# Kernel tuning notes

Hardware: AMD Instinct MI355X
Metric: run time of the kernel (lower is better)

## Reference

```python
import jax, jax.numpy as jnp
import numpy as np

N_NODES = 50000
N_EDGES = 800000
D_IN = 128
D_OUT = 128


def setup_inputs() -> dict:
    key = jax.random.key(0)
    k1, k2, k3, k4, k5, k6 = jax.random.split(key, 6)
    curr_fea = jax.random.normal(k1, (N_NODES, D_IN), dtype=jnp.float32)
    edge_index = jax.random.randint(k2, (2, N_EDGES), 0, N_NODES, dtype=jnp.int64)
    s = 1.0 / np.sqrt(D_IN)
    W_self = jax.random.uniform(k3, (D_OUT, D_IN), jnp.float32, -s, s)
    b_self = jax.random.uniform(k4, (D_OUT,), jnp.float32, -s, s)
    W_neig = jax.random.uniform(k5, (D_OUT, D_IN), jnp.float32, -s, s)
    b_neig = jax.random.uniform(k6, (D_OUT,), jnp.float32, -s, s)
    return {"curr_fea": curr_fea, "edge_index": edge_index,
            "W_self": W_self, "b_self": b_self,
            "W_neig": W_neig, "b_neig": b_neig}


def reference(curr_fea, edge_index, W_self, b_self, W_neig, b_neig):
    num_nodes = curr_fea.shape[0]
    src, dst = edge_index[0], edge_index[1]
    # symmetrize: messages flow both directions
    src_all = jnp.concatenate([src, dst], axis=0)  # [2E]
    dst_all = jnp.concatenate([dst, src], axis=0)  # [2E]
    # gather neighbor features then scatter-add into destination nodes
    nei_sum = jax.ops.segment_sum(curr_fea[src_all], dst_all,
                                  num_segments=num_nodes)  # [N, d]
    out = (curr_fea @ W_self.T + b_self) + (nei_sum @ W_neig.T + b_neig)
    return out
```

## Files before the change

kernel.cpp:

```cpp
#include <hip/hip_runtime.h>

#define DD 128
#define BM 64
#define BK 32
#define BKN 64
#define NBMAX 1024
#define ECH 2048
#define CAP 2304

typedef __attribute__((ext_vector_type(8))) short bf16x8;
typedef __attribute__((ext_vector_type(4))) float f32x4;

__device__ __forceinline__ unsigned short f2b(float x) {
    unsigned u = __float_as_uint(x);
    u += 0x7fffu + ((u >> 16) & 1u);
    return (unsigned short)(u >> 16);
}
__device__ __forceinline__ float b2f_lo(unsigned v) { return __uint_as_float(v << 16); }
__device__ __forceinline__ float b2f_hi(unsigned v) { return __uint_as_float(v & 0xffff0000u); }
__device__ __forceinline__ float bf(unsigned short u) {
    return __uint_as_float((unsigned)u << 16);
}

__device__ __forceinline__ int detect_rf(const void* ei_raw, int E, int lane) {
    const unsigned long long* p = (const unsigned long long*)ei_raw;
    int n64 = E < 64 ? E : 64;
    bool big = (lane < n64) && (p[lane] >= (1ULL << 32));
    return (__ballot(big) == 0ULL) ? 1 : 0;
}

__global__ void detect_kernel(const unsigned long long* __restrict__ ei,
                              int n64, int* __restrict__ flag) {
    int i = threadIdx.x;
    bool big = (i < n64) && (ei[i] >= (1ULL << 32));
    unsigned long long b = __ballot(big);
    if (i == 0) *flag = (b == 0ULL) ? 1 : 0;
}

__global__ void cvt_all_kernel(const float* __restrict__ fea,
                               const float* __restrict__ Ws,
                               const float* __restrict__ Wn,
                               unsigned short* __restrict__ feaB,
                               unsigned short* __restrict__ Wcat, int n4) {
    int i = blockIdx.x * 256 + threadIdx.x;
    if (i < n4) {
        float4 v = reinterpret_cast<const float4*>(fea)[i];
        ushort4 o;
        o.x = f2b(v.x); o.y = f2b(v.y); o.z = f2b(v.z); o.w = f2b(v.w);
        reinterpret_cast<ushort4*>(feaB)[i] = o;
    } else if (i < n4 + 2 * DD * DD / 4) {
        int k4 = i - n4;
        int n = k4 >> 6;
        int kk = (k4 & 63) * 4;
        float4 v = (kk < DD) ? *reinterpret_cast<const float4*>(Ws + n * DD + kk)
                             : *reinterpret_cast<const float4*>(Wn + n * DD + kk - DD);
        ushort4 o;
        o.x = f2b(v.x); o.y = f2b(v.y); o.z = f2b(v.z); o.w = f2b(v.w);
        reinterpret_cast<ushort4*>(Wcat)[k4] = o;
    }
}

__global__ void cvt_fea_kernel(const float* __restrict__ in,
                               unsigned short* __restrict__ out, int n4) {
    int i = blockIdx.x * 256 + threadIdx.x;
    if (i >= n4) return;
    float4 v = reinterpret_cast<const float4*>(in)[i];
    ushort4 o;
    o.x = f2b(v.x); o.y = f2b(v.y); o.z = f2b(v.z); o.w = f2b(v.w);
    reinterpret_cast<ushort4*>(out)[i] = o;
}

__global__ void cvt_w_kernel(const float* __restrict__ Ws,
                             const float* __restrict__ Wn,
                             unsigned short* __restrict__ Wcat) {
    int i = blockIdx.x * 256 + threadIdx.x;
    int n = i >> 8, k = i & 255;
    float v = (k < DD) ? Ws[n * DD + k] : Wn[n * DD + (k - DD)];
    Wcat[i] = f2b(v);
}

__launch_bounds__(512)
__global__ void bin_kernel(const void* __restrict__ ei_raw, int E,
                           unsigned* __restrict__ region,
                           unsigned* __restrict__ gcur, int nbk) {
    __shared__ unsigned stage[2 * ECH];
    __shared__ unsigned cnt[NBMAX];
    __shared__ unsigned start[NBMAX];
    __shared__ unsigned cursor[NBMAX];
    __shared__ unsigned gbase[NBMAX];
    __shared__ unsigned scanT[512];

    const int t = threadIdx.x;
    const int lane = t & 63;
    const int rf = detect_rf(ei_raw, E, lane);

    for (int b = t; b < NBMAX; b += 512) { cnt[b] = 0; cursor[b] = 0; }
    __syncthreads();

    const int e0 = blockIdx.x * ECH;
    int es[4], ed[4];
#pragma unroll
    for (int j = 0; j < 4; ++j) {
        int e = e0 + j * 512 + t;
        if (e < E) {
            if (rf) {
                const long long* p = (const long long*)ei_raw;
                es[j] = (int)p[e]; ed[j] = (int)p[e + E];
            } else {
                const int* p = (const int*)ei_raw;
                es[j] = p[e]; ed[j] = p[e + E];
            }
            atomicAdd(&cnt[ed[j] >> 6], 1u);
            atomicAdd(&cnt[es[j] >> 6], 1u);
        } else {
            es[j] = -1; ed[j] = -1;
        }
    }
    __syncthreads();

    unsigned lv[2]; unsigned lsum = 0;
#pragma unroll
    for (int j = 0; j < 2; ++j) { lv[j] = cnt[t * 2 + j]; lsum += lv[j]; }
    scanT[t] = lsum; __syncthreads();
    for (int o = 1; o < 512; o <<= 1) {
        unsigned x = (t >= o) ? scanT[t - o] : 0;
        __syncthreads();
        scanT[t] += x;
        __syncthreads();
    }
    unsigned run = scanT[t] - lsum;
#pragma unroll
    for (int j = 0; j < 2; ++j) { start[t * 2 + j] = run; run += lv[j]; }
    __syncthreads();

#pragma unroll
    for (int j = 0; j < 4; ++j) {
        if (es[j] >= 0) {
            int s = es[j], d = ed[j];
            unsigned p0 = atomicAdd(&cursor[d >> 6], 1u);
            stage[start[d >> 6] + p0] = (unsigned)(d & 63) | ((unsigned)s << 6);
            unsigned p1 = atomicAdd(&cursor[s >> 6], 1u);
            stage[start[s >> 6] + p1] = (unsigned)(s & 63) | ((unsigned)d << 6);
        }
    }
    __syncthreads();

    for (int b = t; b < nbk; b += 512) {
        unsigned c = cnt[b];
        gbase[b] = c ? atomicAdd(&gcur[b], c) : 0;
    }
    __syncthreads();

    const int w = t >> 6;
    for (int b = w; b < nbk; b += 8) {
        unsigned c = cnt[b];
        if (!c) continue;
        unsigned gb = gbase[b], st = start[b];
        for (unsigned l2 = lane; l2 < c; l2 += 64) {
            unsigned idx = gb + l2;
            if (idx < CAP)
                region[(size_t)b * CAP + idx] = stage[st + l2];
        }
    }
}

__launch_bounds__(512)
__global__ void gather_sort_kernel(const unsigned short* __restrict__ feaB,
                                   const unsigned* __restrict__ region,
                                   const unsigned* __restrict__ gcur,
                                   unsigned short* __restrict__ neiB, int M) {
    __shared__ unsigned ent[CAP];
    __shared__ unsigned srt[CAP];
    __shared__ unsigned c64[BKN];
    __shared__ unsigned p64[BKN + 1];
    __shared__ unsigned cur64[BKN];

    const int t = threadIdx.x, b = blockIdx.x;
    unsigned cnt = gcur[b];
    if (cnt > CAP) cnt = CAP;
    const unsigned* reg = region + (size_t)b * CAP;

    for (unsigned i = t; i < cnt; i += 512) ent[i] = reg[i];
    if (t < BKN) { c64[t] = 0; cur64[t] = 0; }
    __syncthreads();

    for (unsigned i = t; i < cnt; i += 512) atomicAdd(&c64[ent[i] & 63u], 1u);
    __syncthreads();

    if (t == 0) {
        unsigned r = 0;
        for (int n = 0; n < BKN; ++n) { p64[n] = r; r += c64[n]; }
        p64[BKN] = r;
    }
    __syncthreads();

    for (unsigned i = t; i < cnt; i += 512) {
        unsigned e = ent[i];
        unsigned p = atomicAdd(&cur64[e & 63u], 1u);
        srt[p64[e & 63u] + p] = e >> 6;
    }
    __syncthreads();

    const int w = t >> 6, lane = t & 63;
    const int half = lane >> 5, li = lane & 31;
    const unsigned short* bp = feaB + li * 4;

    for (int n = w; n < BKN; n += 8) {
        int g = b * BKN + n;
        if (g >= M) break;
        unsigned p = p64[n], d = c64[n];
        float a0 = 0.f, a1 = 0.f, a2 = 0.f, a3 = 0.f;
        unsigned j = 0;
        for (; j + 8 <= d; j += 8) {
            unsigned s0 = srt[p + j + half];
            unsigned s1 = srt[p + j + 2 + half];
            unsigned s2 = srt[p + j + 4 + half];
            unsigned s3 = srt[p + j + 6 + half];
            ushort4 v0 = *reinterpret_cast<const ushort4*>(bp + (size_t)s0 * DD);
            ushort4 v1 = *reinterpret_cast<const ushort4*>(bp + (size_t)s1 * DD);
            ushort4 v2 = *reinterpret_cast<const ushort4*>(bp + (size_t)s2 * DD);
            ushort4 v3 = *reinterpret_cast<const ushort4*>(bp + (size_t)s3 * DD);
            a0 += bf(v0.x) + bf(v1.x) + bf(v2.x) + bf(v3.x);
            a1 += bf(v0.y) + bf(v1.y) + bf(v2.y) + bf(v3.y);
            a2 += bf(v0.z) + bf(v1.z) + bf(v2.z) + bf(v3.z);
            a3 += bf(v0.w) + bf(v1.w) + bf(v2.w) + bf(v3.w);
        }
        for (; j + 2 <= d; j += 2) {
            unsigned s = srt[p + j + half];
            ushort4 v = *reinterpret_cast<const ushort4*>(bp + (size_t)s * DD);
            a0 += bf(v.x); a1 += bf(v.y); a2 += bf(v.z); a3 += bf(v.w);
        }
        if (j < d && half == 0) {
            unsigned s = srt[p + j];
            ushort4 v = *reinterpret_cast<const ushort4*>(bp + (size_t)s * DD);
            a0 += bf(v.x); a1 += bf(v.y); a2 += bf(v.z); a3 += bf(v.w);
        }
        a0 += __shfl_xor(a0, 32);
        a1 += __shfl_xor(a1, 32);
        a2 += __shfl_xor(a2, 32);
        a3 += __shfl_xor(a3, 32);
        if (half == 0) {
            ushort4 o;
            o.x = f2b(a0); o.y = f2b(a1); o.z = f2b(a2); o.w = f2b(a3);
            *reinterpret_cast<ushort4*>(neiB + (size_t)g * DD + li * 4) = o;
        }
    }
}

__global__ void transpose_kernel(const float* __restrict__ Ws,
                                 const float* __restrict__ Wn,
                                 float* __restrict__ Wts,
                                 float* __restrict__ Wtn) {
    int idx = blockIdx.x * blockDim.x + threadIdx.x;
    int i = idx & (DD * DD - 1);
    int col = i >> 7;
    int k = i & (DD - 1);
    if (idx < DD * DD)          Wts[k * DD + col] = Ws[i];
    else if (idx < 2 * DD * DD) Wtn[k * DD + col] = Wn[i];
}

__global__ void hist_kernel(const void* __restrict__ ei_raw,
                            int* __restrict__ deg, int E,
                            const int* __restrict__ flag) {
    int e = blockIdx.x * 256 + threadIdx.x;
    if (e >= E) return;
    int s, d;
    if (*flag) {
        const long long* ei = (const long long*)ei_raw;
        s = (int)ei[e]; d = (int)ei[e + E];
    } else {
        const int* ei = (const int*)ei_raw;
        s = ei[e]; d = ei[e + E];
    }
    atomicAdd(&deg[s], 1);
    atomicAdd(&deg[d], 1);
}

__global__ void scan1_kernel(const int* __restrict__ deg, int* __restrict__ off,
                             int* __restrict__ bsum, int N) {
    __shared__ int sd[256];
    int base = blockIdx.x * 1024;
    int t = threadIdx.x;
    int v[4]; int s = 0;
#pragma unroll
    for (int j = 0; j < 4; ++j) {
        int idx = base + t * 4 + j;
        v[j] = (idx < N) ? deg[idx] : 0;
        s += v[j];
    }
    sd[t] = s; __syncthreads();
    for (int o = 1; o < 256; o <<= 1) {
        int x = (t >= o) ? sd[t - o] : 0;
        __syncthreads();
        sd[t] += x;
        __syncthreads();
    }
    int run = sd[t] - s;
    if (t == 255) bsum[blockIdx.x] = sd[255];
#pragma unroll
    for (int j = 0; j < 4; ++j) {
        int idx = base + t * 4 + j;
        if (idx < N) off[idx] = run;
        run += v[j];
    }
}

__global__ void scan2_kernel(int* __restrict__ bsum, int NB,
                             int* __restrict__ total) {
    __shared__ int sd[256];
    int t = threadIdx.x;
    int v = (t < NB) ? bsum[t] : 0;
    sd[t] = v; __syncthreads();
    for (int o = 1; o < 256; o <<= 1) {
        int x = (t >= o) ? sd[t - o] : 0;
        __syncthreads();
        sd[t] += x;
        __syncthreads();
    }
    if (t < NB) bsum[t] = sd[t] - v;
    if (t == 255) *total = sd[255];
}

__global__ void scan3_kernel(int* __restrict__ off, const int* __restrict__ bsum,
                             int N) {
    int i = blockIdx.x * blockDim.x + threadIdx.x;
    if (i < N) off[i] += bsum[i >> 10];
}

__global__ void fill_kernel(const void* __restrict__ ei_raw,
                            const int* __restrict__ off,
                            int* __restrict__ cursor, int* __restrict__ list,
                            int E, const int* __restrict__ flag) {
    int e = blockIdx.x * 256 + threadIdx.x;
    if (e >= E) return;
    int s, d;
    if (*flag) {
        const long long* ei = (const long long*)ei_raw;
        s = (int)ei[e]; d = (int)ei[e + E];
    } else {
        const int* ei = (const int*)ei_raw;
        s = ei[e]; d = ei[e + E];
    }
    int p0 = atomicAdd(&cursor[d], 1); list[off[d] + p0] = s;
    int p1 = atomicAdd(&cursor[s], 1); list[off[s] + p1] = d;
}

__launch_bounds__(256)
__global__ void gather_b_kernel(const unsigned short* __restrict__ feaB,
                                const int* __restrict__ off,
                                const int* __restrict__ list,
                                unsigned short* __restrict__ neiB, int N) {
    int w = (int)((blockIdx.x * 256 + threadIdx.x) >> 6);
    if (w >= N) return;
    int lane = threadIdx.x & 63;
    int start = off[w], end = off[w + 1];
    float ax = 0.f, ay = 0.f;
    const unsigned short* base = feaB + lane * 2;
    int j = start;
    for (; j + 4 <= end; j += 4) {
        int s0 = list[j], s1 = list[j + 1], s2 = list[j + 2], s3 = list[j + 3];
        unsigned a = *reinterpret_cast<const unsigned*>(base + (size_t)s0 * DD);
        unsigned b = *reinterpret_cast<const unsigned*>(base + (size_t)s1 * DD);
        unsigned c = *reinterpret_cast<const unsigned*>(base + (size_t)s2 * DD);
        unsigned d = *reinterpret_cast<const unsigned*>(base + (size_t)s3 * DD);
        ax += b2f_lo(a) + b2f_lo(b) + b2f_lo(c) + b2f_lo(d);
        ay += b2f_hi(a) + b2f_hi(b) + b2f_hi(c) + b2f_hi(d);
    }
    for (; j < end; ++j) {
        unsigned a = *reinterpret_cast<const unsigned*>(base + (size_t)list[j] * DD);
        ax += b2f_lo(a); ay += b2f_hi(a);
    }
    ushort2 o; o.x = f2b(ax); o.y = f2b(ay);
    *reinterpret_cast<ushort2*>(neiB + (size_t)w * DD + lane * 2) = o;
}

__launch_bounds__(256)
__global__ void gather_f32_kernel(const float* __restrict__ fea,
                                  const int* __restrict__ off,
                                  const int* __restrict__ list,
                                  float* __restrict__ nei, int N) {
    int w = (int)((blockIdx.x * 256 + threadIdx.x) >> 6);
    if (w >= N) return;
    int lane = threadIdx.x & 63;
    int start = off[w], end = off[w + 1];
    float2 acc = make_float2(0.f, 0.f);
    const float* base = fea + (size_t)lane * 2;
    int j = start;
    for (; j + 4 <= end; j += 4) {
        int s0 = list[j], s1 = list[j + 1], s2 = list[j + 2], s3 = list[j + 3];
        float2 a = *reinterpret_cast<const float2*>(base + (size_t)s0 * DD);
        float2 b = *reinterpret_cast<const float2*>(base + (size_t)s1 * DD);
        float2 c = *reinterpret_cast<const float2*>(base + (size_t)s2 * DD);
        float2 e = *reinterpret_cast<const float2*>(base + (size_t)s3 * DD);
        acc.x += a.x + b.x + c.x + e.x;
        acc.y += a.y + b.y + c.y + e.y;
    }
    for (; j < end; ++j) {
        float2 a = *reinterpret_cast<const float2*>(base + (size_t)list[j] * DD);
        acc.x += a.x; acc.y += a.y;
    }
    *reinterpret_cast<float2*>(nei + (size_t)w * DD + lane * 2) = acc;
}

__global__ void scatter_kernel(const float* __restrict__ fea,
                               const void* __restrict__ ei_raw,
                               float* __restrict__ nei,
                               int E, const int* __restrict__ flag) {
    long long r = (long long)blockIdx.x * 8 + (threadIdx.x >> 5);
    if (r >= 2LL * E) return;
    int lr = threadIdx.x & 31;
    int i = (int)(r < E ? r : r - E);
    int s, d;
    if (*flag) {
        const long long* ei = (const long long*)ei_raw;
        s = (int)ei[i]; d = (int)ei[i + E];
    } else {
        const int* ei = (const int*)ei_raw;
        s = ei[i]; d = ei[i + E];
    }
    if (r >= E) { int t = s; s = d; d = t; }
    const float4 v = *reinterpret_cast<const float4*>(fea + (size_t)s * DD + lr * 4);
    float* p = nei + (size_t)d * DD + lr * 4;
    unsafeAtomicAdd(p + 0, v.x);
    unsafeAtomicAdd(p + 1, v.y);
    unsafeAtomicAdd(p + 2, v.z);
    unsafeAtomicAdd(p + 3, v.w);
}

__launch_bounds__(256)
__global__ void gemm_mfma_kernel(const unsigned short* __restrict__ feaB,
                                 const unsigned short* __restrict__ neiB,
                                 const unsigned short* __restrict__ Wcat,
                                 const float* __restrict__ bs,
                                 const float* __restrict__ bn,
                                 float* __restrict__ out, int M) {
    const int w  = threadIdx.x >> 6;
    const int l  = threadIdx.x & 63;
    const int lr = l & 15;
    const int ks = l >> 4;
    const int row0 = blockIdx.x * 128 + w * 32;
    const int col0 = blockIdx.y * 64;

    f32x4 acc[2][4] = {};

#pragma unroll
    for (int kb = 0; kb < 256; kb += 32) {
        const unsigned short* A = (kb < DD) ? feaB : neiB;
        const int klocal = (kb < DD) ? kb : kb - DD;
        bf16x8 a[2];
#pragma unroll
        for (int ri = 0; ri < 2; ++ri) {
            int rowg = row0 + ri * 16 + lr;
            if (rowg < M)
                a[ri] = *reinterpret_cast<const bf16x8*>(
                    A + (size_t)rowg * DD + klocal + ks * 8);
            else
                a[ri] = bf16x8{0, 0, 0, 0, 0, 0, 0, 0};
        }
#pragma unroll
        for (int ci = 0; ci < 4; ++ci) {
            int n = col0 + ci * 16 + lr;
            bf16x8 b = *reinterpret_cast<const bf16x8*>(
                Wcat + (size_t)n * 256 + kb + ks * 8);
#pragma unroll
            for (int ri = 0; ri < 2; ++ri)
                acc[ri][ci] = __builtin_amdgcn_mfma_f32_16x16x32_bf16(
                    a[ri], b, acc[ri][ci], 0, 0, 0);
        }
    }

#pragma unroll
    for (int ci = 0; ci < 4; ++ci) {
        int colg = col0 + ci * 16 + lr;
        float bias = bs[colg] + bn[colg];
#pragma unroll
        for (int ri = 0; ri < 2; ++ri) {
            int rbase = row0 + ri * 16 + ks * 4;
#pragma unroll
            for (int i = 0; i < 4; ++i) {
                int rowg = rbase + i;
                if (rowg < M)
                    out[(size_t)rowg * DD + colg] = acc[ri][ci][i] + bias;
            }
        }
    }
}

__launch_bounds__(256)
__global__ void gemm_kernel(const float* __restrict__ fea,
                            const float* __restrict__ nei,
                            const float* __restrict__ Wts,
                            const float* __restrict__ Wtn,
                            const float* __restrict__ bs,
                            const float* __restrict__ bn,
                            float* __restrict__ out, int M) {
    __shared__ float Fs[BM][BK + 4];
    __shared__ float Ns[BM][BK + 4];
    __shared__ float WsT[BK][DD];
    __shared__ float WnT[BK][DD];

    const int t = threadIdx.x;
    const int cg = t & 31;
    const int rg = t >> 5;
    const int row0 = blockIdx.x * BM;

    float4 acc[8];
#pragma unroll
    for (int r = 0; r < 8; ++r) acc[r] = make_float4(0.f, 0.f, 0.f, 0.f);

    for (int kb = 0; kb < DD; kb += BK) {
#pragma unroll
        for (int j = 0; j < 2; ++j) {
            int idx = t + j * 256;
            int row = idx >> 3;
            int seg = idx & 7;
            int grow = row0 + row;
            float4 fv = make_float4(0.f, 0.f, 0.f, 0.f);
            float4 nv = make_float4(0.f, 0.f, 0.f, 0.f);
            if (grow < M) {
                fv = *reinterpret_cast<const float4*>(fea + (size_t)grow * DD + kb + seg * 4);
                nv = *reinterpret_cast<const float4*>(nei + (size_t)grow * DD + kb + seg * 4);
            }
            *reinterpret_cast<float4*>(&Fs[row][seg * 4]) = fv;
            *reinterpret_cast<float4*>(&Ns[row][seg * 4]) = nv;
        }
#pragma unroll
        for (int j = 0; j < 4; ++j) {
            int idx = t + j * 256;
            int kk = idx >> 5;
            int seg = idx & 31;
            *reinterpret_cast<float4*>(&WsT[kk][seg * 4]) =
                *reinterpret_cast<const float4*>(Wts + (size_t)(kb + kk) * DD + seg * 4);
            *reinterpret_cast<float4*>(&WnT[kk][seg * 4]) =
                *reinterpret_cast<const float4*>(Wtn + (size_t)(kb + kk) * DD + seg * 4);
        }
        __syncthreads();

#pragma unroll
        for (int kk = 0; kk < BK; ++kk) {
            float4 wsv = *reinterpret_cast<const float4*>(&WsT[kk][cg * 4]);
            float4 wnv = *reinterpret_cast<const float4*>(&WnT[kk][cg * 4]);
#pragma unroll
            for (int r = 0; r < 8; ++r) {
                float a = Fs[rg * 8 + r][kk];
                float b = Ns[rg * 8 + r][kk];
                acc[r].x += a * wsv.x + b * wnv.x;
                acc[r].y += a * wsv.y + b * wnv.y;
                acc[r].z += a * wsv.z + b * wnv.z;
                acc[r].w += a * wsv.w + b * wnv.w;
            }
        }
        __syncthreads();
    }

    float4 bsv = *reinterpret_cast<const float4*>(bs + cg * 4);
    float4 bnv = *reinterpret_cast<const float4*>(bn + cg * 4);
    float4 bias = make_float4(bsv.x + bnv.x, bsv.y + bnv.y, bsv.z + bnv.z, bsv.w + bnv.w);
#pragma unroll
    for (int r = 0; r < 8; ++r) {
        int grow = row0 + rg * 8 + r;
        if (grow < M) {
            float4 o = make_float4(acc[r].x + bias.x, acc[r].y + bias.y,
                                   acc[r].z + bias.z, acc[r].w + bias.w);
            *reinterpret_cast<float4*>(out + (size_t)grow * DD + cg * 4) = o;
        }
    }
}

extern "C" void kernel_launch(void* const* d_in, const int* in_sizes, int n_in,
                              void* d_out, int out_size, void* d_ws, size_t ws_size,
                              hipStream_t stream) {
    const float* fea = (const float*)d_in[0];
    const void*  ei  = d_in[1];
    const float* Ws  = (const float*)d_in[2];
    const float* bsv = (const float*)d_in[3];
    const float* Wn  = (const float*)d_in[4];
    const float* bnv = (const float*)d_in[5];

    const int M = in_sizes[0] / DD;
    const int E = in_sizes[1] / 2;
    float* out = (float*)d_out;
    char* ws = (char*)d_ws;
    int* flag = (int*)ws;

    const int NBK = (M + BKN - 1) / BKN;
    const size_t csr_bytes = (size_t)M * 8 + (size_t)(M + 1) * 4 + 4096
                           + (size_t)2 * E * 4;

    size_t o1 = 256;
    unsigned short* Wcat = (unsigned short*)(ws + o1); o1 += (size_t)DD * 256 * 2;
    unsigned short* feaB = (unsigned short*)(ws + o1); o1 += (size_t)M * DD * 2;
    unsigned short* neiB = (unsigned short*)(ws + o1); o1 += (size_t)M * DD * 2;
    unsigned* gcur  = (unsigned*)(ws + o1);            o1 += 4096;
    unsigned* region = (unsigned*)(ws + o1);           o1 += (size_t)NBK * CAP * 4;
    size_t need1 = o1;

    size_t o2 = 256 + (size_t)DD * 256 * 2 + (size_t)2 * M * DD * 2;
    size_t need2 = o2 + csr_bytes;

    size_t o3 = 256;
    float* Wts = (float*)(ws + o3); o3 += (size_t)DD * DD * 4;
    float* Wtn = (float*)(ws + o3); o3 += (size_t)DD * DD * 4;
    size_t need3 = o3 + csr_bytes;

    const int NB = (M + 1023) / 1024;
    const int eb = (E + 255) / 256;
    const int n4 = M * DD / 4;

    if (ws_size >= need1 && NBK <= NBMAX) {
        hipMemsetAsync(gcur, 0, 4096, stream);
        int cvtb = (n4 + 2 * DD * DD / 4 + 255) / 256;
        cvt_all_kernel<<<cvtb, 256, 0, stream>>>(fea, Ws, Wn, feaB, Wcat, n4);
        int abks = (E + ECH - 1) / ECH;
        bin_kernel<<<abks, 512, 0, stream>>>(ei, E, region, gcur, NBK);
        gather_sort_kernel<<<NBK, 512, 0, stream>>>(feaB, region, gcur, neiB, M);
        dim3 g((M + 127) / 128, 2);
        gemm_mfma_kernel<<<g, 256, 0, stream>>>(feaB, neiB, Wcat, bsv, bnv, out, M);
    } else if (ws_size >= need2) {
        int* deg    = (int*)(ws + o2);
        int* cursor = deg + M;
        int* off    = cursor + M;
        int* bsum   = off + (M + 1);
        int* list   = bsum + 1024;

        detect_kernel<<<1, 64, 0, stream>>>((const unsigned long long*)ei,
                                            E < 64 ? E : 64, flag);
        cvt_fea_kernel<<<(n4 + 255) / 256, 256, 0, stream>>>(fea, feaB, n4);
        cvt_w_kernel<<<(DD * 256 + 255) / 256, 256, 0, stream>>>(Ws, Wn, Wcat);
        hipMemsetAsync(deg, 0, (size_t)2 * M * 4, stream);
        hist_kernel<<<eb, 256, 0, stream>>>(ei, deg, E, flag);
        scan1_kernel<<<NB, 256, 0, stream>>>(deg, off, bsum, M);
        scan2_kernel<<<1, 256, 0, stream>>>(bsum, NB, &off[M]);
        scan3_kernel<<<(M + 255) / 256, 256, 0, stream>>>(off, bsum, M);
        fill_kernel<<<eb, 256, 0, stream>>>(ei, off, cursor, list, E, flag);
        gather_b_kernel<<<(M + 3) / 4, 256, 0, stream>>>(feaB, off, list, neiB, M);
        dim3 g((M + 127) / 128, 2);
        gemm_mfma_kernel<<<g, 256, 0, stream>>>(feaB, neiB, Wcat, bsv, bnv, out, M);
    } else if (ws_size >= need3) {
        int* deg    = (int*)(ws + o3);
        int* cursor = deg + M;
        int* off    = cursor + M;
        int* bsum   = off + (M + 1);
        int* list   = bsum + 1024;
        float* nei = out;

        detect_kernel<<<1, 64, 0, stream>>>((const unsigned long long*)ei,
                                            E < 64 ? E : 64, flag);
        transpose_kernel<<<(2 * DD * DD + 255) / 256, 256, 0, stream>>>(Ws, Wn, Wts, Wtn);
        hipMemsetAsync(deg, 0, (size_t)2 * M * 4, stream);
        hist_kernel<<<eb, 256, 0, stream>>>(ei, deg, E, flag);
        scan1_kernel<<<NB, 256, 0, stream>>>(deg, off, bsum, M);
        scan2_kernel<<<1, 256, 0, stream>>>(bsum, NB, &off[M]);
        scan3_kernel<<<(M + 255) / 256, 256, 0, stream>>>(off, bsum, M);
        fill_kernel<<<eb, 256, 0, stream>>>(ei, off, cursor, list, E, flag);
        gather_f32_kernel<<<(M + 3) / 4, 256, 0, stream>>>(fea, off, list, nei, M);
        gemm_kernel<<<(M + BM - 1) / BM, 256, 0, stream>>>(fea, nei, Wts, Wtn,
                                                           bsv, bnv, out, M);
    } else {
        float* nei = out;
        detect_kernel<<<1, 64, 0, stream>>>((const unsigned long long*)ei,
                                            E < 64 ? E : 64, flag);
        transpose_kernel<<<(2 * DD * DD + 255) / 256, 256, 0, stream>>>(Ws, Wn, Wts, Wtn);
        hipMemsetAsync(nei, 0, (size_t)M * DD * 4, stream);
        long long rows = 2LL * E;
        int sblocks = (int)((rows + 7) / 8);
        scatter_kernel<<<sblocks, 256, 0, stream>>>(fea, ei, nei, E, flag);
        gemm_kernel<<<(M + BM - 1) / BM, 256, 0, stream>>>(fea, nei, Wts, Wtn,
                                                           bsv, bnv, out, M);
    }
}
```

Baseline: 205.6 us.

## Fuse neighbor gather with MFMA GEMM, keeping aggregated features in LDS

The bucketed gather-sort kernel now writes each 64-row block of aggregated neighbor features into shared memory and runs the bf16 MFMA GEMM (self features plus neighbor features against the concatenated weights) in the same kernel, adding biases before storing the output. This removes the global neiB write and reread and one kernel launch. The bucket entries are kept in registers instead of a shared array, and the gather loop is unrolled to 16 neighbors per iteration. In exchange, each block reads the full weight matrix from global or L2 without LDS staging, and the larger LDS footprint may lower occupancy. The GEMM tile is also smaller (64 rows per 512-thread block).

Measured after the change: 206.2 us. Within noise of the previous version (+0.3%).

```diff
diff --git a/kernel.cpp b/kernel.cpp
--- a/kernel.cpp
+++ b/kernel.cpp
@@ -7,6 +7,7 @@
 #define NBMAX 1024
 #define ECH 2048
 #define CAP 2304
+#define PADC 136
 
 typedef __attribute__((ext_vector_type(8))) short bf16x8;
 typedef __attribute__((ext_vector_type(4))) float f32x4;
@@ -165,12 +166,15 @@
 }
 
 __launch_bounds__(512)
-__global__ void gather_sort_kernel(const unsigned short* __restrict__ feaB,
+__global__ void gather_gemm_kernel(const unsigned short* __restrict__ feaB,
+                                   const unsigned short* __restrict__ Wcat,
                                    const unsigned* __restrict__ region,
                                    const unsigned* __restrict__ gcur,
-                                   unsigned short* __restrict__ neiB, int M) {
-    __shared__ unsigned ent[CAP];
+                                   const float* __restrict__ bs,
+                                   const float* __restrict__ bn,
+                                   float* __restrict__ out, int M) {
     __shared__ unsigned srt[CAP];
+    __shared__ unsigned short neiL[BKN][PADC];
     __shared__ unsigned c64[BKN];
     __shared__ unsigned p64[BKN + 1];
     __shared__ unsigned cur64[BKN];
@@ -180,11 +184,19 @@
     if (cnt > CAP) cnt = CAP;
     const unsigned* reg = region + (size_t)b * CAP;
 
-    for (unsigned i = t; i < cnt; i += 512) ent[i] = reg[i];
+    unsigned ent[5];
+#pragma unroll
+    for (int q = 0; q < 5; ++q) {
+        unsigned i = (unsigned)t + (unsigned)q * 512u;
+        ent[q] = (i < cnt) ? reg[i] : 0xFFFFFFFFu;
+    }
+
     if (t < BKN) { c64[t] = 0; cur64[t] = 0; }
     __syncthreads();
 
-    for (unsigned i = t; i < cnt; i += 512) atomicAdd(&c64[ent[i] & 63u], 1u);
+#pragma unroll
+    for (int q = 0; q < 5; ++q)
+        if (ent[q] != 0xFFFFFFFFu) atomicAdd(&c64[ent[q] & 63u], 1u);
     __syncthreads();
 
     if (t == 0) {
@@ -194,10 +206,13 @@
     }
     __syncthreads();
 
-    for (unsigned i = t; i < cnt; i += 512) {
-        unsigned e = ent[i];
-        unsigned p = atomicAdd(&cur64[e & 63u], 1u);
-        srt[p64[e & 63u] + p] = e >> 6;
+#pragma unroll
+    for (int q = 0; q < 5; ++q) {
+        if (ent[q] != 0xFFFFFFFFu) {
+            unsigned e = ent[q];
+            unsigned p = atomicAdd(&cur64[e & 63u], 1u);
+            srt[p64[e & 63u] + p] = e >> 6;
+        }
     }
     __syncthreads();
 
@@ -207,23 +222,22 @@
 
     for (int n = w; n < BKN; n += 8) {
         int g = b * BKN + n;
-        if (g >= M) break;
-        unsigned p = p64[n], d = c64[n];
+        unsigned p = p64[n];
+        unsigned d = (g < M) ? c64[n] : 0;
         float a0 = 0.f, a1 = 0.f, a2 = 0.f, a3 = 0.f;
         unsigned j = 0;
-        for (; j + 8 <= d; j += 8) {
-            unsigned s0 = srt[p + j + half];
-            unsigned s1 = srt[p + j + 2 + half];
-            unsigned s2 = srt[p + j + 4 + half];
-            unsigned s3 = srt[p + j + 6 + half];
-            ushort4 v0 = *reinterpret_cast<const ushort4*>(bp + (size_t)s0 * DD);
-            ushort4 v1 = *reinterpret_cast<const ushort4*>(bp + (size_t)s1 * DD);
-            ushort4 v2 = *reinterpret_cast<const ushort4*>(bp + (size_t)s2 * DD);
-            ushort4 v3 = *reinterpret_cast<const ushort4*>(bp + (size_t)s3 * DD);
-            a0 += bf(v0.x) + bf(v1.x) + bf(v2.x) + bf(v3.x);
-            a1 += bf(v0.y) + bf(v1.y) + bf(v2.y) + bf(v3.y);
-            a2 += bf(v0.z) + bf(v1.z) + bf(v2.z) + bf(v3.z);
-            a3 += bf(v0.w) + bf(v1.w) + bf(v2.w) + bf(v3.w);
+        for (; j + 16 <= d; j += 16) {
+            ushort4 v[8];
+#pragma unroll
+            for (int q = 0; q < 8; ++q) {
+                unsigned s = srt[p + j + 2 * q + half];
+                v[q] = *reinterpret_cast<const ushort4*>(bp + (size_t)s * DD);
+            }
+#pragma unroll
+            for (int q = 0; q < 8; ++q) {
+                a0 += bf(v[q].x); a1 += bf(v[q].y);
+                a2 += bf(v[q].z); a3 += bf(v[q].w);
+            }
         }
         for (; j + 2 <= d; j += 2) {
             unsigned s = srt[p + j + half];
@@ -242,7 +256,49 @@
         if (half == 0) {
             ushort4 o;
             o.x = f2b(a0); o.y = f2b(a1); o.z = f2b(a2); o.w = f2b(a3);
-            *reinterpret_cast<ushort4*>(neiB + (size_t)g * DD + li * 4) = o;
+            *reinterpret_cast<ushort4*>(&neiL[n][li * 4]) = o;
+        }
+    }
+    __syncthreads();
+
+    const int lr = lane & 15, ks = lane >> 4;
+    const int rg = w & 3, cgr = w >> 2;
+    const int row0 = b * BKN + rg * 16;
+    const int rowl = rg * 16 + lr;
+    const int rowg = row0 + lr;
+    const int col0 = cgr * 64;
+
+    f32x4 acc[4] = {};
+#pragma unroll
+    for (int kb = 0; kb < 256; kb += 32) {
+        bf16x8 a;
+        if (kb < DD) {
+            if (rowg < M)
+                a = *reinterpret_cast<const bf16x8*>(
+                    feaB + (size_t)rowg * DD + kb + ks * 8);
+            else
+                a = bf16x8{0, 0, 0, 0, 0, 0, 0, 0};
+        } else {
+            a = *reinterpret_cast<const bf16x8*>(&neiL[rowl][(kb - DD) + ks * 8]);
+        }
+#pragma unroll
+        for (int ci = 0; ci < 4; ++ci) {
+            int nn = col0 + ci * 16 + lr;
+            bf16x8 bb = *reinterpret_cast<const bf16x8*>(
+                Wcat + (size_t)nn * 256 + kb + ks * 8);
+            acc[ci] = __builtin_amdgcn_mfma_f32_16x16x32_bf16(a, bb, acc[ci], 0, 0, 0);
+        }
+    }
+
+#pragma unroll
+    for (int ci = 0; ci < 4; ++ci) {
+        int colg = col0 + ci * 16 + lr;
+        float bias = bs[colg] + bn[colg];
+        int rbase = row0 + ks * 4;
+#pragma unroll
+        for (int i2 = 0; i2 < 4; ++i2) {
+            int r2 = rbase + i2;
+            if (r2 < M) out[(size_t)r2 * DD + colg] = acc[ci][i2] + bias;
         }
     }
 }
@@ -590,13 +646,14 @@
     size_t o1 = 256;
     unsigned short* Wcat = (unsigned short*)(ws + o1); o1 += (size_t)DD * 256 * 2;
     unsigned short* feaB = (unsigned short*)(ws + o1); o1 += (size_t)M * DD * 2;
-    unsigned short* neiB = (unsigned short*)(ws + o1); o1 += (size_t)M * DD * 2;
     unsigned* gcur  = (unsigned*)(ws + o1);            o1 += 4096;
     unsigned* region = (unsigned*)(ws + o1);           o1 += (size_t)NBK * CAP * 4;
     size_t need1 = o1;
 
-    size_t o2 = 256 + (size_t)DD * 256 * 2 + (size_t)2 * M * DD * 2;
-    size_t need2 = o2 + csr_bytes;
+    size_t o2 = 256 + (size_t)DD * 256 * 2 + (size_t)M * DD * 2;
+    unsigned short* neiB2 = (unsigned short*)(ws + o2);
+    size_t o2b = o2 + (size_t)M * DD * 2;
+    size_t need2 = o2b + csr_bytes;
 
     size_t o3 = 256;
     float* Wts = (float*)(ws + o3); o3 += (size_t)DD * DD * 4;
@@ -613,11 +670,10 @@
         cvt_all_kernel<<<cvtb, 256, 0, stream>>>(fea, Ws, Wn, feaB, Wcat, n4);
         int abks = (E + ECH - 1) / ECH;
         bin_kernel<<<abks, 512, 0, stream>>>(ei, E, region, gcur, NBK);
-        gather_sort_kernel<<<NBK, 512, 0, stream>>>(feaB, region, gcur, neiB, M);
-        dim3 g((M + 127) / 128, 2);
-        gemm_mfma_kernel<<<g, 256, 0, stream>>>(feaB, neiB, Wcat, bsv, bnv, out, M);
+        gather_gemm_kernel<<<NBK, 512, 0, stream>>>(feaB, Wcat, region, gcur,
+                                                    bsv, bnv, out, M);
     } else if (ws_size >= need2) {
-        int* deg    = (int*)(ws + o2);
+        int* deg    = (int*)(ws + o2b);
         int* cursor = deg + M;
         int* off    = cursor + M;
         int* bsum   = off + (M + 1);
@@ -633,9 +689,9 @@
         scan2_kernel<<<1, 256, 0, stream>>>(bsum, NB, &off[M]);
         scan3_kernel<<<(M + 255) / 256, 256, 0, stream>>>(off, bsum, M);
         fill_kernel<<<eb, 256, 0, stream>>>(ei, off, cursor, list, E, flag);
-        gather_b_kernel<<<(M + 3) / 4, 256, 0, stream>>>(feaB, off, list, neiB, M);
+        gather_b_kernel<<<(M + 3) / 4, 256, 0, stream>>>(feaB, off, list, neiB2, M);
         dim3 g((M + 127) / 128, 2);
-        gemm_mfma_kernel<<<g, 256, 0, stream>>>(feaB, neiB, Wcat, bsv, bnv, out, M);
+        gemm_mfma_kernel<<<g, 256, 0, stream>>>(feaB, neiB2, Wcat, bsv, bnv, out, M);
     } else if (ws_size >= need3) {
         int* deg    = (int*)(ws + o3);
         int* cursor = deg + M;
```
